# Optimization experiments

Measured on AMD Instinct MI355X. Metric: run time of the kernel, lower is better.

## Reference

```python
import jax, jax.numpy as jnp
import numpy as np


def setup_inputs() -> dict:
    key = jax.random.key(0)
    ks = jax.random.split(key, 5)
    B, T, D, U = 32, 2048, 512, 512
    scale = 1.0 / np.sqrt(D)
    return {
        "full": jax.random.normal(ks[0], (B, T, D), jnp.float32),
        "last": jax.random.normal(ks[1], (B, D), jnp.float32),
        "W1": jax.random.normal(ks[2], (D, U), jnp.float32) * scale,
        "b1": jnp.zeros((U,), jnp.float32),
        "W2": jax.random.normal(ks[3], (D, U), jnp.float32) * scale,
        "b2": jnp.zeros((U,), jnp.float32),
        "V": jax.random.normal(ks[4], (U, 1), jnp.float32) * (1.0 / np.sqrt(U)),
        "bV": jnp.zeros((1,), jnp.float32),
    }


def reference(full, last, W1, b1, W2, b2, V, bV):
    # full: [B,T,D], last: [B,D]
    h1 = jnp.einsum("btd,du->btu", full, W1) + b1          # [B,T,U]
    h2 = last @ W2 + b2                                      # [B,U]
    score = jnp.tanh(h1 + h2[:, None, :]) @ V + bV           # [B,T,1]
    attn = jax.nn.softmax(score, axis=1)                     # [B,T,1]
    context = jnp.sum(attn * full, axis=1)                   # [B,D]
    return context
```

## Files before the change

### kernel.cpp

```cpp
#include <hip/hip_runtime.h>
#include <math.h>


#define BB 32
#define TT 2048
#define DD 512
#define UU 512
#define BKK 32
#define KSTEPS 16

typedef short bf16x8 __attribute__((ext_vector_type(8)));
typedef short s16x4  __attribute__((ext_vector_type(4)));
typedef float f32x4  __attribute__((ext_vector_type(4)));

static __device__ __forceinline__ short f2bf(float f) {
    unsigned x = __float_as_uint(f);
    return (short)((x + 0x7fffu + ((x >> 16) & 1u)) >> 16);
}

static __device__ __forceinline__ float fast_tanh(float x) {
    float e = __expf(2.f * x);
    return 1.f - 2.f * __builtin_amdgcn_rcpf(e + 1.f);
}

__global__ __launch_bounds__(256) void prep_kernel(const float* __restrict__ W1,
                                                   short* __restrict__ W1T,
                                                   const float* __restrict__ last,
                                                   const float* __restrict__ W2,
                                                   const float* __restrict__ b1,
                                                   const float* __restrict__ b2,
                                                   float* __restrict__ h2) {
    __shared__ float tile[32][33];
    __shared__ float ls[DD];
    __shared__ float part[256];
    const int bid = blockIdx.x;
    const int tid = threadIdx.x;
    if (bid < 256) {
        const int tr = (bid >> 4) << 5;
        const int tc = (bid & 15) << 5;
#pragma unroll
        for (int p = 0; p < 4; ++p) {
            const int r = p * 8 + (tid >> 5), c = tid & 31;
            tile[r][c] = W1[(size_t)(tr + r) * UU + tc + c];
        }
        __syncthreads();
#pragma unroll
        for (int p = 0; p < 4; ++p) {
            const int r = p * 8 + (tid >> 5), c = tid & 31;
            W1T[(size_t)(tc + r) * DD + tr + c] = f2bf(tile[c][r]);
        }
    } else {
        const int b2i = bid - 256;
        const int b  = b2i >> 2;
        const int u0 = (b2i & 3) << 7;
        for (int i = tid; i < DD; i += 256) ls[i] = last[b * DD + i];
        __syncthreads();
        const int uu = tid & 127;
        const int dh = tid >> 7;
        float acc = 0.f;
#pragma unroll 8
        for (int d = dh * 256; d < dh * 256 + 256; ++d)
            acc += ls[d] * W2[d * UU + u0 + uu];
        part[tid] = acc;
        __syncthreads();
        if (tid < 128) {
            const int u = u0 + tid;
            h2[b * UU + u] = part[tid] + part[tid + 128] + b1[u] + b2[u];
        }
    }
}

__global__ __launch_bounds__(1024, 4) void score_kernel(const float* __restrict__ full,
                                                        const short* __restrict__ W1T,
                                                        const float* __restrict__ h2,
                                                        const float* __restrict__ V,
                                                        float* __restrict__ ctx,
                                                        float* __restrict__ m_arr,
                                                        float* __restrict__ l_arr) {
    __shared__ __align__(16) short a16[2][128 * 32];
    __shared__ __align__(16) short blds[2][512 * 32];
    __shared__ float red64[16][64];
    __shared__ float esc[128];
    __shared__ float sred[8];
    __shared__ __align__(16) float red4[8][128][4];

    const int bid = blockIdx.x;
    const int b    = bid >> 4;
    const int t0   = (bid & 15) << 7;
    const int tid  = threadIdx.x;
    const int w    = tid >> 6;
    const int lane = tid & 63;
    const int quad = lane >> 4;
    const int col  = lane & 15;
    const int wm   = w >> 3;
    const int wn   = w & 7;

    f32x4 acc[4][4];
#pragma unroll
    for (int i = 0; i < 4; ++i)
#pragma unroll
        for (int j = 0; j < 4; ++j) acc[i][j] = (f32x4){0.f, 0.f, 0.f, 0.f};

    const size_t fullbase = (size_t)(b * TT + t0) * DD;

    const int sr = tid >> 3;
    const int se = tid & 7;
    const float* aSrc = &full[fullbase + (size_t)sr * DD + se * 4];
    const int awOff = sr * 32 + ((((se >> 1) ^ (sr & 3)) << 3) + ((se & 1) << 2));

#define STAGE_B(bufidx, koidx) do {                                                   \
        _Pragma("unroll")                                                             \
        for (int i = 0; i < 2; ++i) {                                                 \
            const int sb = w * 128 + i * 64;                                          \
            const int s  = sb + lane;                                                 \
            const int u  = s >> 2;                                                    \
            const int kc = (s & 3) ^ ((u >> 1) & 3);                                  \
            const short* g = &W1T[(size_t)u * DD + (koidx) * BKK + kc * 8];           \
            __builtin_amdgcn_global_load_lds(                                         \
                (const __attribute__((address_space(1))) void*)g,                     \
                (__attribute__((address_space(3))) void*)&blds[bufidx][sb * 8], 16, 0, 0); \
        }                                                                             \
    } while (0)

#define CVT_WRITE(buf, ar) do {                                                       \
        s16x4 q_ = (s16x4){f2bf((ar).x), f2bf((ar).y), f2bf((ar).z), f2bf((ar).w)};   \
        *(s16x4*)&a16[buf][awOff] = q_;                                               \
    } while (0)

    f32x4 aregA = *(const f32x4*)(aSrc + 0 * BKK);
    f32x4 aregB = *(const f32x4*)(aSrc + 1 * BKK);
    STAGE_B(0, 0);
    STAGE_B(1, 1);
    asm volatile("s_waitcnt vmcnt(5)" ::: "memory");
    CVT_WRITE(0, aregA);
    asm volatile("s_waitcnt vmcnt(2)" ::: "memory");
    asm volatile("s_waitcnt lgkmcnt(0)" ::: "memory");
    __builtin_amdgcn_s_barrier();

    for (int ko = 0; ko < KSTEPS; ++ko) {
        const int cur = ko & 1;
        bf16x8 af[4], bfr[4];
#pragma unroll
        for (int mt = 0; mt < 4; ++mt) {
            const int r = wm * 64 + mt * 16 + col;
            af[mt] = *(const bf16x8*)&a16[cur][r * 32 + ((quad ^ (r & 3)) << 3)];
        }
#pragma unroll
        for (int nt = 0; nt < 4; ++nt) {
            const int u = wn * 64 + nt * 16 + col;
            bfr[nt] = *(const bf16x8*)&blds[cur][(u * 4 + (quad ^ ((u >> 1) & 3))) * 8];
        }
        asm volatile("s_waitcnt lgkmcnt(0)" ::: "memory");
        __builtin_amdgcn_sched_barrier(0);
        __builtin_amdgcn_s_barrier();

        if (ko + 1 < KSTEPS) {
            asm volatile("s_waitcnt vmcnt(2)" ::: "memory");
            if (ko & 1) CVT_WRITE(cur ^ 1, aregA);
            else        CVT_WRITE(cur ^ 1, aregB);
        }
        if (ko + 2 < KSTEPS) {
            if (ko & 1) aregB = *(const f32x4*)(aSrc + (ko + 2) * BKK);
            else        aregA = *(const f32x4*)(aSrc + (ko + 2) * BKK);
        }
        if (ko + 2 < KSTEPS) STAGE_B(cur, ko + 2);

#pragma unroll
        for (int nt = 0; nt < 4; ++nt)
#pragma unroll
            for (int mt = 0; mt < 4; ++mt)
                acc[mt][nt] = __builtin_amdgcn_mfma_f32_16x16x32_bf16(af[mt], bfr[nt], acc[mt][nt], 0, 0, 0);

        if (ko < KSTEPS - 2) {
            asm volatile("s_waitcnt vmcnt(3)" ::: "memory");
        } else if (ko == KSTEPS - 2) {
            asm volatile("s_waitcnt vmcnt(0)" ::: "memory");
        }
        if (ko < KSTEPS - 1) {
            asm volatile("s_waitcnt lgkmcnt(0)" ::: "memory");
            __builtin_amdgcn_s_barrier();
        }
    }
#undef STAGE_B
#undef CVT_WRITE

    float srow[16];
#pragma unroll
    for (int i = 0; i < 16; ++i) srow[i] = 0.f;
#pragma unroll
    for (int nt = 0; nt < 4; ++nt) {
        const int u = wn * 64 + nt * 16 + col;
        const float hv = h2[b * UU + u];
        const float vv = V[u];
#pragma unroll
        for (int mt = 0; mt < 4; ++mt)
#pragma unroll
            for (int r = 0; r < 4; ++r)
                srow[mt * 4 + r] += fast_tanh(acc[mt][nt][r] + hv) * vv;
    }
#pragma unroll
    for (int off = 1; off < 16; off <<= 1) {
#pragma unroll
        for (int i = 0; i < 16; ++i) srow[i] += __shfl_xor(srow[i], off, 64);
    }
    if (col == 0) {
#pragma unroll
        for (int mt = 0; mt < 4; ++mt)
#pragma unroll
            for (int r = 0; r < 4; ++r)
                red64[w][mt * 16 + quad * 4 + r] = srow[mt * 4 + r];
    }
    __syncthreads();

    float sv = 0.f;
    if (tid < 128) {
        const int wmX = tid >> 6, rr = tid & 63;
#pragma unroll
        for (int j = 0; j < 8; ++j) sv += red64[wmX * 8 + j][rr];
        float mv = sv;
#pragma unroll
        for (int off = 1; off < 64; off <<= 1) mv = fmaxf(mv, __shfl_xor(mv, off, 64));
        if (lane == 0) sred[w] = mv;
    }
    __syncthreads();
    const float M = fmaxf(sred[0], sred[1]);
    if (tid < 128) {
        float e = __expf(sv - M);
        esc[tid] = e;
#pragma unroll
        for (int off = 1; off < 64; off <<= 1) e += __shfl_xor(e, off, 64);
        if (lane == 0) sred[4 + w] = e;
    }
    __syncthreads();
    if (tid == 0) { m_arr[bid] = M; l_arr[bid] = sred[4] + sred[5]; }

    const int c  = tid & 127;
    const int tp = tid >> 7;
    float ax = 0.f, ay = 0.f, az = 0.f, aw = 0.f;
#pragma unroll 4
    for (int i = 0; i < 16; ++i) {
        const int t = i * 8 + tp;
        const float4 v = *(const float4*)&full[fullbase + (size_t)t * DD + c * 4];
        const float e = esc[t];
        ax += e * v.x; ay += e * v.y; az += e * v.z; aw += e * v.w;
    }
    *(float4*)&red4[tp][c][0] = make_float4(ax, ay, az, aw);
    __syncthreads();
    if (tp == 0) {
        float4 s = make_float4(0.f, 0.f, 0.f, 0.f);
#pragma unroll
        for (int j = 0; j < 8; ++j) {
            const float4 p = *(const float4*)&red4[j][c][0];
            s.x += p.x; s.y += p.y; s.z += p.z; s.w += p.w;
        }
        *(float4*)&ctx[(size_t)bid * DD + c * 4] = s;
    }
}

__global__ __launch_bounds__(256) void combine_kernel(const float* __restrict__ ctx,
                                                      const float* __restrict__ m_arr,
                                                      const float* __restrict__ l_arr,
                                                      float* __restrict__ out) {
    const int b = blockIdx.x;
    const int tid = threadIdx.x;
    __shared__ float wgt[16];
    __shared__ float linv;
    if (tid == 0) {
        float M = -1e30f;
#pragma unroll
        for (int i = 0; i < 16; ++i) M = fmaxf(M, m_arr[b * 16 + i]);
        float l = 0.f;
#pragma unroll
        for (int i = 0; i < 16; ++i) {
            wgt[i] = __expf(m_arr[b * 16 + i] - M);
            l += wgt[i] * l_arr[b * 16 + i];
        }
        linv = 1.f / l;
    }
    __syncthreads();
    float s0 = 0.f, s1 = 0.f;
#pragma unroll
    for (int i = 0; i < 16; ++i) {
        const float wi = wgt[i];
        const float* cp = &ctx[(size_t)(b * 16 + i) * DD + tid * 2];
        s0 += wi * cp[0];
        s1 += wi * cp[1];
    }
    out[b * DD + tid * 2]     = s0 * linv;
    out[b * DD + tid * 2 + 1] = s1 * linv;
}

extern "C" void kernel_launch(void* const* d_in, const int* in_sizes, int n_in,
                              void* d_out, int out_size, void* d_ws, size_t ws_size,
                              hipStream_t stream) {
    const float* full = (const float*)d_in[0];
    const float* last = (const float*)d_in[1];
    const float* W1   = (const float*)d_in[2];
    const float* b1   = (const float*)d_in[3];
    const float* W2   = (const float*)d_in[4];
    const float* b2   = (const float*)d_in[5];
    const float* V    = (const float*)d_in[6];

    float* out   = (float*)d_out;
    float* h2    = (float*)d_ws;
    float* m_arr = h2 + (size_t)BB * UU;
    float* l_arr = m_arr + 512;
    float* ctx   = l_arr + 512;
    short* W1T   = (short*)(ctx + (size_t)BB * 16 * DD);

    prep_kernel<<<384, 256, 0, stream>>>(W1, W1T, last, W2, b1, b2, h2);
    score_kernel<<<BB * 16, 1024, 0, stream>>>(full, W1T, h2, V, ctx, m_arr, l_arr);
    combine_kernel<<<BB, 256, 0, stream>>>(ctx, m_arr, l_arr, out);
}
```

Measured before the change: 266.7 us.

## Halve score block size and process rows in two halves with online softmax merge

```diff
diff --git a/kernel.cpp b/kernel.cpp
--- a/kernel.cpp
+++ b/kernel.cpp
@@ -70,21 +70,23 @@
     }
 }
 
-__global__ __launch_bounds__(1024, 4) void score_kernel(const float* __restrict__ full,
-                                                        const short* __restrict__ W1T,
-                                                        const float* __restrict__ h2,
-                                                        const float* __restrict__ V,
-                                                        float* __restrict__ ctx,
-                                                        float* __restrict__ m_arr,
-                                                        float* __restrict__ l_arr) {
-    __shared__ __align__(16) short a16[2][128 * 32];
-    __shared__ __align__(16) short blds[2][512 * 32];
-    __shared__ float red64[16][64];
-    __shared__ float esc[128];
-    __shared__ float sred[8];
-    __shared__ __align__(16) float red4[8][128][4];
-
-    const int bid = blockIdx.x;
+__global__ __launch_bounds__(512, 4) void score_kernel(const float* __restrict__ full,
+                                                       const short* __restrict__ W1T,
+                                                       const float* __restrict__ h2,
+                                                       const float* __restrict__ V,
+                                                       float* __restrict__ ctx,
+                                                       float* __restrict__ m_arr,
+                                                       float* __restrict__ l_arr) {
+    __shared__ __align__(16) char smem[71712];
+    short* a16  = (short*)smem;
+    short* blds = (short*)(smem + 4096);
+    float* ctxH = (float*)(smem + 4096 + 65536);
+    float* mlh  = (float*)(smem + 4096 + 65536 + 2048);
+    float (*red64)[64]    = (float(*)[64])(smem + 4096);
+    float* esc            = (float*)(smem + 4096 + 2048);
+    float (*red4)[128][4] = (float(*)[128][4])(smem + 4096 + 2304);
+
+    const int bid  = blockIdx.x;
     const int b    = bid >> 4;
     const int t0   = (bid & 15) << 7;
     const int tid  = threadIdx.x;
@@ -92,169 +94,180 @@
     const int lane = tid & 63;
     const int quad = lane >> 4;
     const int col  = lane & 15;
-    const int wm   = w >> 3;
-    const int wn   = w & 7;
-
-    f32x4 acc[4][4];
-#pragma unroll
-    for (int i = 0; i < 4; ++i)
-#pragma unroll
-        for (int j = 0; j < 4; ++j) acc[i][j] = (f32x4){0.f, 0.f, 0.f, 0.f};
-
-    const size_t fullbase = (size_t)(b * TT + t0) * DD;
 
     const int sr = tid >> 3;
     const int se = tid & 7;
-    const float* aSrc = &full[fullbase + (size_t)sr * DD + se * 4];
     const int awOff = sr * 32 + ((((se >> 1) ^ (sr & 3)) << 3) + ((se & 1) << 2));
 
 #define STAGE_B(bufidx, koidx) do {                                                   \
         _Pragma("unroll")                                                             \
-        for (int i = 0; i < 2; ++i) {                                                 \
-            const int sb = w * 128 + i * 64;                                          \
+        for (int i = 0; i < 4; ++i) {                                                 \
+            const int sb = w * 256 + i * 64;                                          \
             const int s  = sb + lane;                                                 \
             const int u  = s >> 2;                                                    \
             const int kc = (s & 3) ^ ((u >> 1) & 3);                                  \
             const short* g = &W1T[(size_t)u * DD + (koidx) * BKK + kc * 8];           \
             __builtin_amdgcn_global_load_lds(                                         \
                 (const __attribute__((address_space(1))) void*)g,                     \
-                (__attribute__((address_space(3))) void*)&blds[bufidx][sb * 8], 16, 0, 0); \
+                (__attribute__((address_space(3))) void*)&blds[(bufidx) * 16384 + sb * 8], 16, 0, 0); \
         }                                                                             \
     } while (0)
 
-#define CVT_WRITE(buf, ar) do {                                                       \
+#define CVT_WRITE(ar) do {                                                            \
         s16x4 q_ = (s16x4){f2bf((ar).x), f2bf((ar).y), f2bf((ar).z), f2bf((ar).w)};   \
-        *(s16x4*)&a16[buf][awOff] = q_;                                               \
+        *(s16x4*)&a16[awOff] = q_;                                                    \
     } while (0)
 
-    f32x4 aregA = *(const f32x4*)(aSrc + 0 * BKK);
-    f32x4 aregB = *(const f32x4*)(aSrc + 1 * BKK);
-    STAGE_B(0, 0);
-    STAGE_B(1, 1);
-    asm volatile("s_waitcnt vmcnt(5)" ::: "memory");
-    CVT_WRITE(0, aregA);
-    asm volatile("s_waitcnt vmcnt(2)" ::: "memory");
-    asm volatile("s_waitcnt lgkmcnt(0)" ::: "memory");
-    __builtin_amdgcn_s_barrier();
-
-    for (int ko = 0; ko < KSTEPS; ++ko) {
-        const int cur = ko & 1;
-        bf16x8 af[4], bfr[4];
-#pragma unroll
-        for (int mt = 0; mt < 4; ++mt) {
-            const int r = wm * 64 + mt * 16 + col;
-            af[mt] = *(const bf16x8*)&a16[cur][r * 32 + ((quad ^ (r & 3)) << 3)];
-        }
+    for (int h = 0; h < 2; ++h) {
+        const size_t rowbase = (size_t)(b * TT + t0 + h * 64) * DD;
+        const float* aSrc = &full[rowbase + (size_t)sr * DD + se * 4];
+
+        f32x4 acc[4][4];
+#pragma unroll
+        for (int i = 0; i < 4; ++i)
+#pragma unroll
+            for (int j = 0; j < 4; ++j) acc[i][j] = (f32x4){0.f, 0.f, 0.f, 0.f};
+
+        f32x4 aregA = *(const f32x4*)(aSrc + 0 * BKK);
+        f32x4 aregB = *(const f32x4*)(aSrc + 1 * BKK);
+        __builtin_amdgcn_sched_barrier(0);
+        STAGE_B(0, 0);
+        STAGE_B(1, 1);
+        __builtin_amdgcn_sched_barrier(0);
+        asm volatile("s_waitcnt vmcnt(9)" ::: "memory");
+        CVT_WRITE(aregA);
+        asm volatile("s_waitcnt vmcnt(4)" ::: "memory");
+        asm volatile("s_waitcnt lgkmcnt(0)" ::: "memory");
+        __builtin_amdgcn_s_barrier();
+
+        for (int ko = 0; ko < KSTEPS; ++ko) {
+            const int cur = ko & 1;
+            bf16x8 af[4], bfr[4];
+#pragma unroll
+            for (int mt = 0; mt < 4; ++mt) {
+                const int r = mt * 16 + col;
+                af[mt] = *(const bf16x8*)&a16[r * 32 + ((quad ^ (r & 3)) << 3)];
+            }
+#pragma unroll
+            for (int nt = 0; nt < 4; ++nt) {
+                const int u = w * 64 + nt * 16 + col;
+                bfr[nt] = *(const bf16x8*)&blds[cur * 16384 + (u * 4 + (quad ^ ((u >> 1) & 3))) * 8];
+            }
+            asm volatile("s_waitcnt lgkmcnt(0)" ::: "memory");
+            __builtin_amdgcn_sched_barrier(0);
+            __builtin_amdgcn_s_barrier();
+
+            if (ko + 1 < KSTEPS) {
+                asm volatile("s_waitcnt vmcnt(4)" ::: "memory");
+                if (ko & 1) CVT_WRITE(aregA);
+                else        CVT_WRITE(aregB);
+            }
+            if (ko + 2 < KSTEPS) {
+                if (ko & 1) aregB = *(const f32x4*)(aSrc + (ko + 2) * BKK);
+                else        aregA = *(const f32x4*)(aSrc + (ko + 2) * BKK);
+            }
+            if (ko + 2 < KSTEPS) STAGE_B(cur, ko + 2);
+
+#pragma unroll
+            for (int nt = 0; nt < 4; ++nt)
+#pragma unroll
+                for (int mt = 0; mt < 4; ++mt)
+                    acc[mt][nt] = __builtin_amdgcn_mfma_f32_16x16x32_bf16(af[mt], bfr[nt], acc[mt][nt], 0, 0, 0);
+
+            if (ko < KSTEPS - 2) {
+                asm volatile("s_waitcnt vmcnt(5)" ::: "memory");
+            } else if (ko == KSTEPS - 2) {
+                asm volatile("s_waitcnt vmcnt(0)" ::: "memory");
+            }
+            if (ko < KSTEPS - 1) {
+                asm volatile("s_waitcnt lgkmcnt(0)" ::: "memory");
+                __builtin_amdgcn_s_barrier();
+            }
+        }
+
+        float srow[16];
+#pragma unroll
+        for (int i = 0; i < 16; ++i) srow[i] = 0.f;
 #pragma unroll
         for (int nt = 0; nt < 4; ++nt) {
-            const int u = wn * 64 + nt * 16 + col;
-            bfr[nt] = *(const bf16x8*)&blds[cur][(u * 4 + (quad ^ ((u >> 1) & 3))) * 8];
-        }
-        asm volatile("s_waitcnt lgkmcnt(0)" ::: "memory");
-        __builtin_amdgcn_sched_barrier(0);
-        __builtin_amdgcn_s_barrier();
-
-        if (ko + 1 < KSTEPS) {
-            asm volatile("s_waitcnt vmcnt(2)" ::: "memory");
-            if (ko & 1) CVT_WRITE(cur ^ 1, aregA);
-            else        CVT_WRITE(cur ^ 1, aregB);
-        }
-        if (ko + 2 < KSTEPS) {
-            if (ko & 1) aregB = *(const f32x4*)(aSrc + (ko + 2) * BKK);
-            else        aregA = *(const f32x4*)(aSrc + (ko + 2) * BKK);
-        }
-        if (ko + 2 < KSTEPS) STAGE_B(cur, ko + 2);
-
-#pragma unroll
-        for (int nt = 0; nt < 4; ++nt)
+            const int u = w * 64 + nt * 16 + col;
+            const float hv = h2[b * UU + u];
+            const float vv = V[u];
 #pragma unroll
             for (int mt = 0; mt < 4; ++mt)
-                acc[mt][nt] = __builtin_amdgcn_mfma_f32_16x16x32_bf16(af[mt], bfr[nt], acc[mt][nt], 0, 0, 0);
-
-        if (ko < KSTEPS - 2) {
-            asm volatile("s_waitcnt vmcnt(3)" ::: "memory");
-        } else if (ko == KSTEPS - 2) {
-            asm volatile("s_waitcnt vmcnt(0)" ::: "memory");
-        }
-        if (ko < KSTEPS - 1) {
-            asm volatile("s_waitcnt lgkmcnt(0)" ::: "memory");
-            __builtin_amdgcn_s_barrier();
-        }
+#pragma unroll
+                for (int r = 0; r < 4; ++r)
+                    srow[mt * 4 + r] += fast_tanh(acc[mt][nt][r] + hv) * vv;
+        }
+#pragma unroll
+        for (int off = 1; off < 16; off <<= 1) {
+#pragma unroll
+            for (int i = 0; i < 16; ++i) srow[i] += __shfl_xor(srow[i], off, 64);
+        }
+        __syncthreads();
+        if (col == 0) {
+#pragma unroll
+            for (int mt = 0; mt < 4; ++mt)
+#pragma unroll
+                for (int r = 0; r < 4; ++r)
+                    red64[w][mt * 16 + quad * 4 + r] = srow[mt * 4 + r];
+        }
+        __syncthreads();
+
+        if (tid < 64) {
+            float sv = 0.f;
+#pragma unroll
+            for (int j = 0; j < 8; ++j) sv += red64[j][lane];
+            float mv = sv;
+#pragma unroll
+            for (int off = 1; off < 64; off <<= 1) mv = fmaxf(mv, __shfl_xor(mv, off, 64));
+            float e = __expf(sv - mv);
+            esc[lane] = e;
+            float l = e;
+#pragma unroll
+            for (int off = 1; off < 64; off <<= 1) l += __shfl_xor(l, off, 64);
+            if (lane == 0) { mlh[h * 2] = mv; mlh[h * 2 + 1] = l; }
+        }
+        __syncthreads();
+
+        const int c  = tid & 127;
+        const int tp = tid >> 7;
+        float ax = 0.f, ay = 0.f, az = 0.f, aw = 0.f;
+#pragma unroll 4
+        for (int i = 0; i < 16; ++i) {
+            const int t = i * 4 + tp;
+            const float4 v = *(const float4*)&full[rowbase + (size_t)t * DD + c * 4];
+            const float e = esc[t];
+            ax += e * v.x; ay += e * v.y; az += e * v.z; aw += e * v.w;
+        }
+        *(float4*)&red4[tp][c][0] = make_float4(ax, ay, az, aw);
+        __syncthreads();
+        if (tp == 0) {
+            const float4 p0 = *(const float4*)&red4[0][c][0];
+            const float4 p1 = *(const float4*)&red4[1][c][0];
+            const float4 p2 = *(const float4*)&red4[2][c][0];
+            const float4 p3 = *(const float4*)&red4[3][c][0];
+            float4 s = make_float4(p0.x + p1.x + p2.x + p3.x,
+                                   p0.y + p1.y + p2.y + p3.y,
+                                   p0.z + p1.z + p2.z + p3.z,
+                                   p0.w + p1.w + p2.w + p3.w);
+            if (h == 0) {
+                *(float4*)&ctxH[c * 4] = s;
+            } else {
+                const float m0 = mlh[0], l0 = mlh[1], m1 = mlh[2], l1 = mlh[3];
+                const float M  = fmaxf(m0, m1);
+                const float w0 = __expf(m0 - M), w1 = __expf(m1 - M);
+                const float4 p = *(const float4*)&ctxH[c * 4];
+                float4 o = make_float4(w0 * p.x + w1 * s.x, w0 * p.y + w1 * s.y,
+                                       w0 * p.z + w1 * s.z, w0 * p.w + w1 * s.w);
+                *(float4*)&ctx[(size_t)bid * DD + c * 4] = o;
+                if (tid == 0) { m_arr[bid] = M; l_arr[bid] = w0 * l0 + w1 * l1; }
+            }
+        }
+        __syncthreads();
     }
 #undef STAGE_B
 #undef CVT_WRITE
-
-    float srow[16];
-#pragma unroll
-    for (int i = 0; i < 16; ++i) srow[i] = 0.f;
-#pragma unroll
-    for (int nt = 0; nt < 4; ++nt) {
-        const int u = wn * 64 + nt * 16 + col;
-        const float hv = h2[b * UU + u];
-        const float vv = V[u];
-#pragma unroll
-        for (int mt = 0; mt < 4; ++mt)
-#pragma unroll
-            for (int r = 0; r < 4; ++r)
-                srow[mt * 4 + r] += fast_tanh(acc[mt][nt][r] + hv) * vv;
-    }
-#pragma unroll
-    for (int off = 1; off < 16; off <<= 1) {
-#pragma unroll
-        for (int i = 0; i < 16; ++i) srow[i] += __shfl_xor(srow[i], off, 64);
-    }
-    if (col == 0) {
-#pragma unroll
-        for (int mt = 0; mt < 4; ++mt)
-#pragma unroll
-            for (int r = 0; r < 4; ++r)
-                red64[w][mt * 16 + quad * 4 + r] = srow[mt * 4 + r];
-    }
-    __syncthreads();
-
-    float sv = 0.f;
-    if (tid < 128) {
-        const int wmX = tid >> 6, rr = tid & 63;
-#pragma unroll
-        for (int j = 0; j < 8; ++j) sv += red64[wmX * 8 + j][rr];
-        float mv = sv;
-#pragma unroll
-        for (int off = 1; off < 64; off <<= 1) mv = fmaxf(mv, __shfl_xor(mv, off, 64));
-        if (lane == 0) sred[w] = mv;
-    }
-    __syncthreads();
-    const float M = fmaxf(sred[0], sred[1]);
-    if (tid < 128) {
-        float e = __expf(sv - M);
-        esc[tid] = e;
-#pragma unroll
-        for (int off = 1; off < 64; off <<= 1) e += __shfl_xor(e, off, 64);
-        if (lane == 0) sred[4 + w] = e;
-    }
-    __syncthreads();
-    if (tid == 0) { m_arr[bid] = M; l_arr[bid] = sred[4] + sred[5]; }
-
-    const int c  = tid & 127;
-    const int tp = tid >> 7;
-    float ax = 0.f, ay = 0.f, az = 0.f, aw = 0.f;
-#pragma unroll 4
-    for (int i = 0; i < 16; ++i) {
-        const int t = i * 8 + tp;
-        const float4 v = *(const float4*)&full[fullbase + (size_t)t * DD + c * 4];
-        const float e = esc[t];
-        ax += e * v.x; ay += e * v.y; az += e * v.z; aw += e * v.w;
-    }
-    *(float4*)&red4[tp][c][0] = make_float4(ax, ay, az, aw);
-    __syncthreads();
-    if (tp == 0) {
-        float4 s = make_float4(0.f, 0.f, 0.f, 0.f);
-#pragma unroll
-        for (int j = 0; j < 8; ++j) {
-            const float4 p = *(const float4*)&red4[j][c][0];
-            s.x += p.x; s.y += p.y; s.z += p.z; s.w += p.w;
-        }
-        *(float4*)&ctx[(size_t)bid * DD + c * 4] = s;
-    }
 }
 
 __global__ __launch_bounds__(256) void combine_kernel(const float* __restrict__ ctx,
@@ -309,6 +322,6 @@
     short* W1T   = (short*)(ctx + (size_t)BB * 16 * DD);
 
     prep_kernel<<<384, 256, 0, stream>>>(W1, W1T, last, W2, b1, b2, h2);
-    score_kernel<<<BB * 16, 1024, 0, stream>>>(full, W1T, h2, V, ctx, m_arr, l_arr);
+    score_kernel<<<BB * 16, 512, 0, stream>>>(full, W1T, h2, V, ctx, m_arr, l_arr);
     combine_kernel<<<BB, 256, 0, stream>>>(ctx, m_arr, l_arr, out);
 }
```

New measurement: 363.1 us. +36.1%, slower.
